# Kernel optimization log

Hardware: AMD Instinct MI355X
Metric: run time of the kernel (lower is better)

## Reference

```python
import jax, jax.numpy as jnp
import numpy as np

N_NODES = 100000
N_EDGES = 3200000
IN_C = 128
OUT_C = 40
NEG_SLOPE = 0.2


def _p(key, shape, scale=0.1):
    return jax.random.normal(key, shape, dtype=jnp.float32) * scale


def setup_inputs() -> dict:
    key = jax.random.key(0)
    ks = jax.random.split(key, 16)
    x = jax.random.normal(ks[0], (N_NODES, IN_C), dtype=jnp.float32)
    edge_index = jax.random.randint(ks[1], (2, N_EDGES), 0, N_NODES, dtype=jnp.int32)
    # layer 1: in=128 -> heads=4, out=4 (concat -> 16)
    W1 = _p(ks[2], (IN_C, 4 * 4))
    a_src1 = _p(ks[3], (4, 4))
    a_dst1 = _p(ks[4], (4, 4))
    b1 = jnp.zeros((16,), jnp.float32)
    # layer 2: 16 -> heads=8, out=8 (concat -> 64)
    W2 = _p(ks[5], (16, 8 * 8))
    a_src2 = _p(ks[6], (8, 8))
    a_dst2 = _p(ks[7], (8, 8))
    b2 = jnp.zeros((64,), jnp.float32)
    # layer 3: 64 -> heads=1, out=OUT_C, concat=False
    W3 = _p(ks[8], (64, OUT_C))
    a_src3 = _p(ks[9], (1, OUT_C))
    a_dst3 = _p(ks[10], (1, OUT_C))
    b3 = jnp.zeros((OUT_C,), jnp.float32)
    return {"x": x, "edge_index": edge_index,
            "W1": W1, "a_src1": a_src1, "a_dst1": a_dst1, "b1": b1,
            "W2": W2, "a_src2": a_src2, "a_dst2": a_dst2, "b2": b2,
            "W3": W3, "a_src3": a_src3, "a_dst3": a_dst3, "b3": b3}


def gat_conv(x, src, dst, W, a_src, a_dst, b, heads, out_c, concat):
    # x: [N, F_in]; src/dst: [E] (self loops already included)
    N = x.shape[0]
    h = (x @ W).reshape(N, heads, out_c)                 # [N, H, C]
    e_src = jnp.sum(h * a_src, axis=-1)                  # [N, H]
    e_dst = jnp.sum(h * a_dst, axis=-1)                  # [N, H]
    e = jax.nn.leaky_relu(e_src[src] + e_dst[dst], NEG_SLOPE)  # [E, H]
    # segment softmax over edges grouped by destination node
    m = jax.ops.segment_max(e, dst, num_segments=N)      # [N, H]
    ex = jnp.exp(e - m[dst])
    s = jax.ops.segment_sum(ex, dst, num_segments=N)
    alpha = ex / (s[dst] + 1e-16)                        # [E, H]
    out = jax.ops.segment_sum(h[src] * alpha[:, :, None], dst, num_segments=N)  # [N, H, C]
    out = out.reshape(N, heads * out_c) if concat else out.mean(axis=1)
    return out + b


def reference(x, edge_index, W1, a_src1, a_dst1, b1, W2, a_src2, a_dst2, b2, W3, a_src3, a_dst3, b3):
    N = x.shape[0]
    loops = jnp.arange(N, dtype=edge_index.dtype)
    src = jnp.concatenate([edge_index[0], loops])
    dst = jnp.concatenate([edge_index[1], loops])
    h = jax.nn.elu(gat_conv(x, src, dst, W1, a_src1, a_dst1, b1, 4, 4, True))
    h = jax.nn.elu(gat_conv(h, src, dst, W2, a_src2, a_dst2, b2, 8, 8, True))
    out = gat_conv(h, src, dst, W3, a_src3, a_dst3, b3, 1, OUT_C, False)
    return out
```

## Files before the change

kernel.cpp:

```cpp
#include <hip/hip_runtime.h>

#define NN 100000
#define NE 3200000
#define ET (NE + NN)
#define NEG_SLOPE 0.2f
#define BSH 7
#define WIN (1 << BSH)
#define NBUC ((NN + WIN - 1) >> BSH)
#define NBLK 256
#define EPB ((ET + NBLK - 1) / NBLK)

__device__ __forceinline__ float lrelu(float v) { return v > 0.f ? v : NEG_SLOPE * v; }

__device__ __forceinline__ unsigned short f2bf(float x) {
    unsigned u = __float_as_uint(x);
    return (unsigned short)((u + 0x7fffu + ((u >> 16) & 1u)) >> 16);
}
__device__ __forceinline__ float bflo(unsigned u) { return __uint_as_float(u << 16); }
__device__ __forceinline__ float bfhi(unsigned u) { return __uint_as_float(u & 0xffff0000u); }


__global__ __launch_bounds__(256) void cnt_kernel(const int* __restrict__ dst,
                                                  int* __restrict__ cnt) {
    __shared__ int h[NBUC];
    for (int i = threadIdx.x; i < NBUC; i += 256) h[i] = 0;
    __syncthreads();
    int lo = blockIdx.x * EPB;
    int hi = lo + EPB; if (hi > ET) hi = ET;
    for (int k = lo + threadIdx.x; k < hi; k += 256) {
        int d = (k < NE) ? dst[k] : k - NE;
        atomicAdd(&h[d >> BSH], 1);
    }
    __syncthreads();
    for (int i = threadIdx.x; i < NBUC; i += 256)
        cnt[i * NBLK + blockIdx.x] = h[i];
}

__global__ __launch_bounds__(256) void rowsum_kernel(const int* __restrict__ cnt,
                                                     int* __restrict__ tot) {
    int wave = threadIdx.x >> 6, lane = threadIdx.x & 63;
    int b = blockIdx.x * 4 + wave;
    if (b >= NBUC) return;
    int4 v = ((const int4*)(cnt + b * NBLK))[lane];
    int s = v.x + v.y + v.z + v.w;
#pragma unroll
    for (int off = 32; off; off >>= 1) s += __shfl_xor(s, off);
    if (lane == 0) tot[b] = s;
}

__global__ __launch_bounds__(1024) void scan_kernel(const int* __restrict__ tot,
                                                    int* __restrict__ bstart) {
    __shared__ int t[1024];
    int b = threadIdx.x;
    int s = (b < NBUC) ? tot[b] : 0;
    t[b] = s;
    __syncthreads();
    for (int off = 1; off < 1024; off <<= 1) {
        int v = (b >= off) ? t[b - off] : 0;
        __syncthreads();
        t[b] += v;
        __syncthreads();
    }
    if (b < NBUC) bstart[b] = t[b] - s;
    if (b == 0) bstart[NBUC] = ET;
}

__global__ __launch_bounds__(256) void base_kernel(int* __restrict__ cnt,
                                                   const int* __restrict__ bstart) {
    int wave = threadIdx.x >> 6, lane = threadIdx.x & 63;
    int b = blockIdx.x * 4 + wave;
    if (b >= NBUC) return;
    int run = bstart[b];
    for (int c0 = 0; c0 < NBLK; c0 += 64) {
        int v = cnt[b * NBLK + c0 + lane];
        int x = v;
#pragma unroll
        for (int off = 1; off < 64; off <<= 1) {
            int y = __shfl_up(x, off);
            if (lane >= off) x += y;
        }
        cnt[b * NBLK + c0 + lane] = run + x - v;
        run += __shfl(x, 63);
    }
}

__global__ __launch_bounds__(256) void scatter_kernel(const int* __restrict__ src,
                                                      const int* __restrict__ dst,
                                                      const int* __restrict__ base,
                                                      unsigned* __restrict__ tmpp) {
    __shared__ int loff[NBUC];
    for (int i = threadIdx.x; i < NBUC; i += 256) loff[i] = base[i * NBLK + blockIdx.x];
    __syncthreads();
    int lo = blockIdx.x * EPB;
    int hi = lo + EPB; if (hi > ET) hi = ET;
    for (int k = lo + threadIdx.x; k < hi; k += 256) {
        int s, d;
        if (k < NE) { s = src[k]; d = dst[k]; }
        else { s = d = k - NE; }
        int p = atomicAdd(&loff[d >> BSH], 1);
        tmpp[p] = (unsigned)s | ((unsigned)(d & (WIN - 1)) << 17);
    }
}

__global__ __launch_bounds__(256) void sort_kernel(const int* __restrict__ bstart,
                                                   const unsigned* __restrict__ tmpp,
                                                   int* __restrict__ rowptr,
                                                   int* __restrict__ ssrc) {
    __shared__ int hist[WIN];
    __shared__ int scan[WIN];
    __shared__ int cur[WIN];
    int buc = blockIdx.x;
    int nlo = buc << BSH;
    int nwin = NN - nlo; if (nwin > WIN) nwin = WIN;
    int lo = bstart[buc], hi = bstart[buc + 1];
    int tid = threadIdx.x;
    if (tid < WIN) hist[tid] = 0;
    __syncthreads();
    for (int k = lo + tid; k < hi; k += 256)
        atomicAdd(&hist[tmpp[k] >> 17], 1);
    __syncthreads();
    if (tid < WIN) scan[tid] = hist[tid];
    __syncthreads();
    for (int off = 1; off < WIN; off <<= 1) {
        int v = (tid >= off && tid < WIN) ? scan[tid - off] : 0;
        __syncthreads();
        if (tid < WIN) scan[tid] += v;
        __syncthreads();
    }
    if (tid < WIN) {
        int ex = scan[tid] - hist[tid];
        cur[tid] = ex;
        if (tid < nwin) rowptr[nlo + tid] = lo + ex;
    }
    if (buc == 0 && tid == 0) rowptr[NN] = ET;
    __syncthreads();
    for (int k = lo + tid; k < hi; k += 256) {
        unsigned e = tmpp[k];
        int p = atomicAdd(&cur[e >> 17], 1);
        ssrc[lo + p] = (int)(e & 0x1FFFFu);
    }
}


template <int FIN, int FOUT>
__global__ void gemm_kernel(const float* __restrict__ x, const float* __restrict__ W,
                            unsigned short* __restrict__ h, int N) {
    __shared__ float Ws[FIN * FOUT];
    for (int i = threadIdx.x; i < FIN * FOUT; i += blockDim.x) Ws[i] = W[i];
    __syncthreads();
    int idx = blockIdx.x * blockDim.x + threadIdx.x;
    if (idx >= N * FOUT) return;
    int n = idx / FOUT, f = idx - n * FOUT;
    const float* xr = x + (long)n * FIN;
    float a = 0.f;
#pragma unroll 8
    for (int k = 0; k < FIN; ++k) a += xr[k] * Ws[k * FOUT + f];
    h[idx] = f2bf(a);
}

template <int H, int C>
__global__ void attn_kernel(const unsigned short* __restrict__ h,
                            const float* __restrict__ a_src,
                            const float* __restrict__ a_dst, float* __restrict__ esrc,
                            float* __restrict__ edst, int N) {
    int idx = blockIdx.x * blockDim.x + threadIdx.x;
    if (idx >= N * H) return;
    int hh = idx % H;
    const unsigned short* hp = h + (long)idx * C;
    float s = 0.f, d = 0.f;
#pragma unroll
    for (int c = 0; c < C; ++c) {
        float v = bflo((unsigned)hp[c]);
        s += v * a_src[hh * C + c];
        d += v * a_dst[hh * C + c];
    }
    esrc[idx] = s;
    edst[idx] = d;
}

template <int H, int C, int L, int G, int NPW, int FPL, bool ELU>
__global__ __launch_bounds__(256) void agg_kernel(
    const int* __restrict__ rowptr, const int* __restrict__ ssrc,
    const float* __restrict__ esrc, const float* __restrict__ edst,
    const unsigned short* __restrict__ hbuf, const float* __restrict__ b,
    float* __restrict__ out, int N) {
    constexpr int F = H * C;
    constexpr int AQ = F / FPL;
    constexpr int S = L * G;
    static_assert(S * NPW == 64, "wave layout");
    static_assert(AQ <= L, "lanes cover features");
    int lane = threadIdx.x & 63;
    int wave = threadIdx.x >> 6;
    int sub = lane / S;
    int ls = lane - sub * S;
    int g = ls / L, q = ls - g * L;
    int n = (blockIdx.x * 4 + wave) * NPW + sub;
    if (n >= N) return;
    const bool act = (q < AQ);
    int h = act ? (FPL * q) / C : 0;
    int qa = act ? q : 0;
    float edn = edst[n * H + h];
    int beg = rowptr[n], end = rowptr[n + 1];
    float sum = 0.f;
    float acc[FPL];
#pragma unroll
    for (int i = 0; i < FPL; ++i) acc[i] = 0.f;

    auto fetch = [&](int s, float ex) {
        if constexpr (FPL == 8) {
            uint4 u = ((const uint4*)hbuf)[s * AQ + qa];
            acc[0] += ex * bflo(u.x); acc[1] += ex * bfhi(u.x);
            acc[2] += ex * bflo(u.y); acc[3] += ex * bfhi(u.y);
            acc[4] += ex * bflo(u.z); acc[5] += ex * bfhi(u.z);
            acc[6] += ex * bflo(u.w); acc[7] += ex * bfhi(u.w);
        } else {
            uint2 u = ((const uint2*)hbuf)[s * AQ + qa];
            acc[0] += ex * bflo(u.x); acc[1] += ex * bfhi(u.x);
            acc[2] += ex * bflo(u.y); acc[3] += ex * bfhi(u.y);
        }
    };

    int k = beg + g;
    int s_cur = (k < end) ? ssrc[k] : 0;
    while (k + G < end) {
        int s1 = ssrc[k + G];
        float e0 = esrc[s_cur * H + h];
        float e1 = esrc[s1 * H + h];
        float x0 = act ? __expf(lrelu(e0 + edn)) : 0.f;
        float x1 = act ? __expf(lrelu(e1 + edn)) : 0.f;
        fetch(s_cur, x0);
        fetch(s1, x1);
        sum += x0 + x1;
        k += 2 * G;
        s_cur = (k < end) ? ssrc[k] : 0;
    }
    if (k < end) {
        float e0 = esrc[s_cur * H + h];
        float x0 = act ? __expf(lrelu(e0 + edn)) : 0.f;
        fetch(s_cur, x0);
        sum += x0;
    }
#pragma unroll
    for (int step = L; step < S; step <<= 1) {
        sum += __shfl_xor(sum, step);
#pragma unroll
        for (int i = 0; i < FPL; ++i) acc[i] += __shfl_xor(acc[i], step);
    }
    if (g == 0 && act) {
        float inv = 1.f / (sum + 1e-16f);
        float v[FPL];
#pragma unroll
        for (int i = 0; i < FPL; ++i) {
            v[i] = acc[i] * inv + b[FPL * q + i];
            if (ELU) v[i] = v[i] > 0.f ? v[i] : __expf(v[i]) - 1.f;
        }
        float* op = out + n * F + FPL * q;
#pragma unroll
        for (int i = 0; i < FPL; i += 4)
            *(float4*)(op + i) = make_float4(v[i], v[i + 1], v[i + 2], v[i + 3]);
    }
}

static inline int cdiv(long a, int b) { return (int)((a + b - 1) / b); }

extern "C" void kernel_launch(void* const* d_in, const int* in_sizes, int n_in,
                              void* d_out, int out_size, void* d_ws, size_t ws_size,
                              hipStream_t stream) {
    const float* x1 = (const float*)d_in[0];
    const int* ei = (const int*)d_in[1];
    const int* src = ei;
    const int* dst = ei + NE;
    const float* W1 = (const float*)d_in[2];
    const float* as1 = (const float*)d_in[3];
    const float* ad1 = (const float*)d_in[4];
    const float* b1 = (const float*)d_in[5];
    const float* W2 = (const float*)d_in[6];
    const float* as2 = (const float*)d_in[7];
    const float* ad2 = (const float*)d_in[8];
    const float* b2 = (const float*)d_in[9];
    const float* W3 = (const float*)d_in[10];
    const float* as3 = (const float*)d_in[11];
    const float* ad3 = (const float*)d_in[12];
    const float* b3 = (const float*)d_in[13];
    float* out = (float*)d_out;

    char* wsb = (char*)d_ws;
    unsigned short* hbuf = (unsigned short*)wsb;  wsb += (long)NN * 64 * 2;
    float* x2 = (float*)wsb;         wsb += (long)NN * 16 * 4;
    float* x3 = (float*)wsb;         wsb += (long)NN * 64 * 4;
    float* esrc = (float*)wsb;       wsb += (long)NN * 8 * 4;
    float* edst = (float*)wsb;       wsb += (long)NN * 8 * 4;
    unsigned* tmpp = (unsigned*)wsb; wsb += (long)ET * 4;
    int* ssrc = (int*)wsb;           wsb += (long)ET * 4;
    int* rowptr = (int*)wsb;         wsb += (long)(NN + 1) * 4;
    int* cnt = (int*)wsb;            wsb += (long)NBUC * NBLK * 4;
    int* bstart = (int*)wsb;         wsb += (long)(NBUC + 1) * 4;
    int* tot = (int*)wsb;            wsb += (long)NBUC * 4;

    const int B = 256;

    cnt_kernel<<<NBLK, B, 0, stream>>>(dst, cnt);
    rowsum_kernel<<<cdiv(NBUC, 4), B, 0, stream>>>(cnt, tot);
    scan_kernel<<<1, 1024, 0, stream>>>(tot, bstart);
    base_kernel<<<cdiv(NBUC, 4), B, 0, stream>>>(cnt, bstart);
    scatter_kernel<<<NBLK, B, 0, stream>>>(src, dst, cnt, tmpp);
    sort_kernel<<<NBUC, B, 0, stream>>>(bstart, tmpp, rowptr, ssrc);

    gemm_kernel<128, 16><<<cdiv((long)NN * 16, B), B, 0, stream>>>(x1, W1, hbuf, NN);
    attn_kernel<4, 4><<<cdiv((long)NN * 4, B), B, 0, stream>>>(hbuf, as1, ad1, esrc, edst, NN);
    agg_kernel<4, 4, 4, 8, 2, 4, true><<<cdiv(NN, 8), B, 0, stream>>>(rowptr, ssrc, esrc, edst, hbuf, b1, x2, NN);

    gemm_kernel<16, 64><<<cdiv((long)NN * 64, B), B, 0, stream>>>(x2, W2, hbuf, NN);
    attn_kernel<8, 8><<<cdiv((long)NN * 8, B), B, 0, stream>>>(hbuf, as2, ad2, esrc, edst, NN);
    agg_kernel<8, 8, 8, 8, 1, 8, true><<<cdiv(NN, 4), B, 0, stream>>>(rowptr, ssrc, esrc, edst, hbuf, b2, x3, NN);

    gemm_kernel<64, 40><<<cdiv((long)NN * 40, B), B, 0, stream>>>(x3, W3, hbuf, NN);
    attn_kernel<1, 40><<<cdiv((long)NN * 1, B), B, 0, stream>>>(hbuf, as3, ad3, esrc, edst, NN);
    agg_kernel<1, 40, 8, 8, 1, 8, false><<<cdiv(NN, 4), B, 0, stream>>>(rowptr, ssrc, esrc, edst, hbuf, b3, out, NN);
}
```

Before: 521.0 us.

## Fuse GEMM with attention logits, pad layer-3 rows, deepen gather unroll

Layers 1 and 2 now compute the per-head attention logits inside the GEMM kernel with a lane shuffle reduction, which removes the separate attention kernels and the extra read of h. Layer 3 stores h with a row stride of 64 bf16 values, giving aligned 16-byte row chunks. The aggregation loop is rewritten to issue U independent index, feature and logit loads before the accumulation, exposing more memory-level parallelism. The cost is higher register pressure in the aggregation kernel and a larger, padded layer-3 buffer.

```diff
diff --git a/kernel.cpp b/kernel.cpp
--- a/kernel.cpp
+++ b/kernel.cpp
@@ -142,9 +142,13 @@
 }
 
 
-template <int FIN, int FOUT>
-__global__ void gemm_kernel(const float* __restrict__ x, const float* __restrict__ W,
-                            unsigned short* __restrict__ h, int N) {
+template <int FIN, int FOUT, int C>
+__global__ __launch_bounds__(256) void gemm_attn_kernel(
+    const float* __restrict__ x, const float* __restrict__ W,
+    const float* __restrict__ a_src, const float* __restrict__ a_dst,
+    unsigned short* __restrict__ h, float* __restrict__ esrc,
+    float* __restrict__ edst, int N) {
+    constexpr int HH = FOUT / C;
     __shared__ float Ws[FIN * FOUT];
     for (int i = threadIdx.x; i < FIN * FOUT; i += blockDim.x) Ws[i] = W[i];
     __syncthreads();
@@ -155,30 +159,59 @@
     float a = 0.f;
 #pragma unroll 8
     for (int k = 0; k < FIN; ++k) a += xr[k] * Ws[k * FOUT + f];
-    h[idx] = f2bf(a);
-}
-
-template <int H, int C>
+    unsigned short ab = f2bf(a);
+    h[idx] = ab;
+    float aq = bflo((unsigned)ab);
+    float vs = aq * a_src[f];
+    float vd = aq * a_dst[f];
+#pragma unroll
+    for (int off = 1; off < C; off <<= 1) {
+        vs += __shfl_xor(vs, off);
+        vd += __shfl_xor(vd, off);
+    }
+    if ((f & (C - 1)) == 0) {
+        int hh = f / C;
+        esrc[n * HH + hh] = vs;
+        edst[n * HH + hh] = vd;
+    }
+}
+
+template <int FIN, int FOUT, int SO>
+__global__ void gemm_kernel(const float* __restrict__ x, const float* __restrict__ W,
+                            unsigned short* __restrict__ h, int N) {
+    __shared__ float Ws[FIN * FOUT];
+    for (int i = threadIdx.x; i < FIN * FOUT; i += blockDim.x) Ws[i] = W[i];
+    __syncthreads();
+    int idx = blockIdx.x * blockDim.x + threadIdx.x;
+    if (idx >= N * FOUT) return;
+    int n = idx / FOUT, f = idx - n * FOUT;
+    const float* xr = x + (long)n * FIN;
+    float a = 0.f;
+#pragma unroll 8
+    for (int k = 0; k < FIN; ++k) a += xr[k] * Ws[k * FOUT + f];
+    h[n * SO + f] = f2bf(a);
+}
+
+template <int C, int SO>
 __global__ void attn_kernel(const unsigned short* __restrict__ h,
                             const float* __restrict__ a_src,
                             const float* __restrict__ a_dst, float* __restrict__ esrc,
                             float* __restrict__ edst, int N) {
     int idx = blockIdx.x * blockDim.x + threadIdx.x;
-    if (idx >= N * H) return;
-    int hh = idx % H;
-    const unsigned short* hp = h + (long)idx * C;
+    if (idx >= N) return;
+    const unsigned short* hp = h + (long)idx * SO;
     float s = 0.f, d = 0.f;
 #pragma unroll
     for (int c = 0; c < C; ++c) {
         float v = bflo((unsigned)hp[c]);
-        s += v * a_src[hh * C + c];
-        d += v * a_dst[hh * C + c];
+        s += v * a_src[c];
+        d += v * a_dst[c];
     }
     esrc[idx] = s;
     edst[idx] = d;
 }
 
-template <int H, int C, int L, int G, int NPW, int FPL, bool ELU>
+template <int H, int C, int L, int G, int NPW, int FPL, int RSL, int U, bool ELU>
 __global__ __launch_bounds__(256) void agg_kernel(
     const int* __restrict__ rowptr, const int* __restrict__ ssrc,
     const float* __restrict__ esrc, const float* __restrict__ edst,
@@ -206,39 +239,55 @@
 #pragma unroll
     for (int i = 0; i < FPL; ++i) acc[i] = 0.f;
 
-    auto fetch = [&](int s, float ex) {
+    int k = beg + g;
+    while (k + (U - 1) * G < end) {
+        int ss[U];
+#pragma unroll
+        for (int u = 0; u < U; ++u) ss[u] = ssrc[k + u * G];
+        uint4 hv4[U];
+        uint2 hv2[U];
+#pragma unroll
+        for (int u = 0; u < U; ++u) {
+            if constexpr (FPL == 8) hv4[u] = ((const uint4*)hbuf)[ss[u] * RSL + qa];
+            else hv2[u] = ((const uint2*)hbuf)[ss[u] * RSL + qa];
+        }
+        float es[U];
+#pragma unroll
+        for (int u = 0; u < U; ++u) es[u] = esrc[ss[u] * H + h];
+#pragma unroll
+        for (int u = 0; u < U; ++u) {
+            float ex = act ? __expf(lrelu(es[u] + edn)) : 0.f;
+            if constexpr (FPL == 8) {
+                uint4 v = hv4[u];
+                acc[0] += ex * bflo(v.x); acc[1] += ex * bfhi(v.x);
+                acc[2] += ex * bflo(v.y); acc[3] += ex * bfhi(v.y);
+                acc[4] += ex * bflo(v.z); acc[5] += ex * bfhi(v.z);
+                acc[6] += ex * bflo(v.w); acc[7] += ex * bfhi(v.w);
+            } else {
+                uint2 v = hv2[u];
+                acc[0] += ex * bflo(v.x); acc[1] += ex * bfhi(v.x);
+                acc[2] += ex * bflo(v.y); acc[3] += ex * bfhi(v.y);
+            }
+            sum += ex;
+        }
+        k += U * G;
+    }
+    while (k < end) {
+        int s0 = ssrc[k];
+        float ex = act ? __expf(lrelu(esrc[s0 * H + h] + edn)) : 0.f;
         if constexpr (FPL == 8) {
-            uint4 u = ((const uint4*)hbuf)[s * AQ + qa];
-            acc[0] += ex * bflo(u.x); acc[1] += ex * bfhi(u.x);
-            acc[2] += ex * bflo(u.y); acc[3] += ex * bfhi(u.y);
-            acc[4] += ex * bflo(u.z); acc[5] += ex * bfhi(u.z);
-            acc[6] += ex * bflo(u.w); acc[7] += ex * bfhi(u.w);
+            uint4 v = ((const uint4*)hbuf)[s0 * RSL + qa];
+            acc[0] += ex * bflo(v.x); acc[1] += ex * bfhi(v.x);
+            acc[2] += ex * bflo(v.y); acc[3] += ex * bfhi(v.y);
+            acc[4] += ex * bflo(v.z); acc[5] += ex * bfhi(v.z);
+            acc[6] += ex * bflo(v.w); acc[7] += ex * bfhi(v.w);
         } else {
-            uint2 u = ((const uint2*)hbuf)[s * AQ + qa];
-            acc[0] += ex * bflo(u.x); acc[1] += ex * bfhi(u.x);
-            acc[2] += ex * bflo(u.y); acc[3] += ex * bfhi(u.y);
-        }
-    };
-
-    int k = beg + g;
-    int s_cur = (k < end) ? ssrc[k] : 0;
-    while (k + G < end) {
-        int s1 = ssrc[k + G];
-        float e0 = esrc[s_cur * H + h];
-        float e1 = esrc[s1 * H + h];
-        float x0 = act ? __expf(lrelu(e0 + edn)) : 0.f;
-        float x1 = act ? __expf(lrelu(e1 + edn)) : 0.f;
-        fetch(s_cur, x0);
-        fetch(s1, x1);
-        sum += x0 + x1;
-        k += 2 * G;
-        s_cur = (k < end) ? ssrc[k] : 0;
-    }
-    if (k < end) {
-        float e0 = esrc[s_cur * H + h];
-        float x0 = act ? __expf(lrelu(e0 + edn)) : 0.f;
-        fetch(s_cur, x0);
-        sum += x0;
+            uint2 v = ((const uint2*)hbuf)[s0 * RSL + qa];
+            acc[0] += ex * bflo(v.x); acc[1] += ex * bfhi(v.x);
+            acc[2] += ex * bflo(v.y); acc[3] += ex * bfhi(v.y);
+        }
+        sum += ex;
+        k += G;
     }
 #pragma unroll
     for (int step = L; step < S; step <<= 1) {
@@ -306,15 +355,18 @@
     scatter_kernel<<<NBLK, B, 0, stream>>>(src, dst, cnt, tmpp);
     sort_kernel<<<NBUC, B, 0, stream>>>(bstart, tmpp, rowptr, ssrc);
 
-    gemm_kernel<128, 16><<<cdiv((long)NN * 16, B), B, 0, stream>>>(x1, W1, hbuf, NN);
-    attn_kernel<4, 4><<<cdiv((long)NN * 4, B), B, 0, stream>>>(hbuf, as1, ad1, esrc, edst, NN);
-    agg_kernel<4, 4, 4, 8, 2, 4, true><<<cdiv(NN, 8), B, 0, stream>>>(rowptr, ssrc, esrc, edst, hbuf, b1, x2, NN);
-
-    gemm_kernel<16, 64><<<cdiv((long)NN * 64, B), B, 0, stream>>>(x2, W2, hbuf, NN);
-    attn_kernel<8, 8><<<cdiv((long)NN * 8, B), B, 0, stream>>>(hbuf, as2, ad2, esrc, edst, NN);
-    agg_kernel<8, 8, 8, 8, 1, 8, true><<<cdiv(NN, 4), B, 0, stream>>>(rowptr, ssrc, esrc, edst, hbuf, b2, x3, NN);
-
-    gemm_kernel<64, 40><<<cdiv((long)NN * 40, B), B, 0, stream>>>(x3, W3, hbuf, NN);
-    attn_kernel<1, 40><<<cdiv((long)NN * 1, B), B, 0, stream>>>(hbuf, as3, ad3, esrc, edst, NN);
-    agg_kernel<1, 40, 8, 8, 1, 8, false><<<cdiv(NN, 4), B, 0, stream>>>(rowptr, ssrc, esrc, edst, hbuf, b3, out, NN);
-}
+    gemm_attn_kernel<128, 16, 4><<<cdiv((long)NN * 16, B), B, 0, stream>>>(
+        x1, W1, as1, ad1, hbuf, esrc, edst, NN);
+    agg_kernel<4, 4, 4, 8, 2, 4, 4, 4, true><<<cdiv(NN, 8), B, 0, stream>>>(
+        rowptr, ssrc, esrc, edst, hbuf, b1, x2, NN);
+
+    gemm_attn_kernel<16, 64, 8><<<cdiv((long)NN * 64, B), B, 0, stream>>>(
+        x2, W2, as2, ad2, hbuf, esrc, edst, NN);
+    agg_kernel<8, 8, 8, 8, 1, 8, 8, 4, true><<<cdiv(NN, 4), B, 0, stream>>>(
+        rowptr, ssrc, esrc, edst, hbuf, b2, x3, NN);
+
+    gemm_kernel<64, 40, 64><<<cdiv((long)NN * 40, B), B, 0, stream>>>(x3, W3, hbuf, NN);
+    attn_kernel<40, 64><<<cdiv(NN, B), B, 0, stream>>>(hbuf, as3, ad3, esrc, edst, NN);
+    agg_kernel<1, 40, 8, 8, 1, 8, 8, 2, false><<<cdiv(NN, 4), B, 0, stream>>>(
+        rowptr, ssrc, esrc, edst, hbuf, b3, out, NN);
+}
```

After: 520.7 us. No clear change (-0.1%).
